# Optimization experiments

Hardware: AMD Instinct MI355X
Metric: run time of the kernel (lower is better)

Reference implementation:

```python
import jax, jax.numpy as jnp
import numpy as np

B, N = 4, 4096
CIN, COUT = 64, 64
K, R, BOX = 3, 32, 4
MLP = COUT * 4
HEADS = 4
EPS = 0.0


def setup_inputs() -> dict:
    key = jax.random.key(0)
    ks = jax.random.split(key, 16)
    s = lambda i, shape: jax.random.normal(ks[i], shape, jnp.float32) * 0.05
    return dict(
        features=jax.random.normal(ks[0], (B, CIN, N), jnp.float32),
        coords=jax.random.normal(ks[1], (B, 3, N), jnp.float32),
        conv_w=s(2, (COUT, CIN, K, K, K)), conv_b=jnp.zeros((COUT,), jnp.float32),
        ln1_g=jnp.ones((COUT,), jnp.float32), ln1_b=jnp.zeros((COUT,), jnp.float32),
        qkv_w=s(3, (3 * COUT, COUT)), qkv_b=jnp.zeros((3 * COUT,), jnp.float32),
        proj_w=s(4, (COUT, COUT)), proj_b=jnp.zeros((COUT,), jnp.float32),
        ln2_g=jnp.ones((COUT,), jnp.float32), ln2_b=jnp.zeros((COUT,), jnp.float32),
        mlp_w1=s(5, (MLP, COUT)), mlp_b1=jnp.zeros((MLP,), jnp.float32),
        mlp_w2=s(6, (COUT, MLP)), mlp_b2=jnp.zeros((COUT,), jnp.float32),
        se_w1=s(7, (COUT // 8, COUT)), se_w2=s(8, (COUT, COUT // 8)),
        pt_in_w=s(9, (COUT, CIN)), pt_in_b=jnp.zeros((COUT,), jnp.float32),
        q_w=s(10, (COUT // 4, COUT)), k_w=s(11, (COUT // 4, COUT)),
        v_w=s(12, (COUT, COUT)),
        trans_w=s(13, (COUT, COUT)), trans_b=jnp.zeros((COUT,), jnp.float32),
    )


def layernorm(x, g, b):
    m = x.mean(-1, keepdims=True)
    v = x.var(-1, keepdims=True)
    return (x - m) * jax.lax.rsqrt(v + 1e-5) * g + b


def voxelize(features, coords):
    # PVCNN-style: center, normalize to [0,1], scale to [0, R-1]; scatter-mean.
    c = coords - coords.mean(axis=2, keepdims=True)  # (B,3,N)
    mx = jnp.sqrt((c ** 2).sum(axis=1, keepdims=True)).max(axis=2, keepdims=True)
    nc = c / (2.0 * mx + EPS) + 0.5
    nc = jnp.clip(nc * R, 0.0, R - 1)  # float coords in [0, R-1]
    vc = jnp.round(nc).astype(jnp.int32)
    idx = (vc[:, 0] * R + vc[:, 1]) * R + vc[:, 2]
    idx = (idx + jnp.arange(B, dtype=jnp.int32)[:, None] * R ** 3).reshape(-1)
    flat = features.transpose(0, 2, 1).reshape(B * N, CIN)
    sums = jax.ops.segment_sum(flat, idx, num_segments=B * R ** 3)
    cnt = jax.ops.segment_sum(jnp.ones((B * N,), jnp.float32), idx, num_segments=B * R ** 3)
    avg = sums / jnp.maximum(cnt, 1.0)[:, None]
    grid = avg.reshape(B, R, R, R, CIN).transpose(0, 4, 1, 2, 3)  # (B,C,R,R,R)
    return grid, nc


def devoxelize(grid, nc):
    # trilinear gather from (B,C,R,R,R) at float coords nc (B,3,N)
    g = grid.reshape(B, COUT, R ** 3)
    x0 = jnp.floor(nc)
    f = nc - x0
    x0 = x0.astype(jnp.int32)
    out = jnp.zeros((B, COUT, N), jnp.float32)
    for dx in (0, 1):
        for dy in (0, 1):
            for dz in (0, 1):
                xi = jnp.clip(x0[:, 0] + dx, 0, R - 1)
                yi = jnp.clip(x0[:, 1] + dy, 0, R - 1)
                zi = jnp.clip(x0[:, 2] + dz, 0, R - 1)
                idx = (xi * R + yi) * R + zi  # (B,N)
                w = ((f[:, 0] if dx else 1 - f[:, 0]) *
                     (f[:, 1] if dy else 1 - f[:, 1]) *
                     (f[:, 2] if dz else 1 - f[:, 2]))
                vals = jnp.take_along_axis(g, jnp.broadcast_to(idx[:, None, :], (B, COUT, N)), axis=2)
                out = out + vals * w[:, None, :]
    return out


def voxel_encoder(grid, conv_w, conv_b, ln1_g, ln1_b, qkv_w, qkv_b, proj_w, proj_b,
                  ln2_g, ln2_b, mlp_w1, mlp_b1, mlp_w2, mlp_b2):
    x = jax.lax.conv_general_dilated(grid, conv_w, (1, 1, 1), 'SAME',
                                     dimension_numbers=('NCDHW', 'OIDHW', 'NCDHW'))
    x = jax.nn.relu(x + conv_b[None, :, None, None, None])
    nb = R // BOX
    # window partition -> (B*nb^3, BOX^3, C)
    t = x.transpose(0, 2, 3, 4, 1).reshape(B, nb, BOX, nb, BOX, nb, BOX, COUT)
    t = t.transpose(0, 1, 3, 5, 2, 4, 6, 7).reshape(B * nb ** 3, BOX ** 3, COUT)
    h = layernorm(t, ln1_g, ln1_b)
    qkv = h @ qkv_w.T + qkv_b
    q, k, v = jnp.split(qkv, 3, axis=-1)
    hd = COUT // HEADS
    sh = lambda z: z.reshape(z.shape[0], z.shape[1], HEADS, hd).transpose(0, 2, 1, 3)
    q, k, v = sh(q), sh(k), sh(v)
    attn = jax.nn.softmax(jnp.einsum('whid,whjd->whij', q, k) / np.float32(np.sqrt(hd)), axis=-1)
    o = jnp.einsum('whij,whjd->whid', attn, v).transpose(0, 2, 1, 3).reshape(t.shape)
    t = t + (o @ proj_w.T + proj_b)
    h = layernorm(t, ln2_g, ln2_b)
    t = t + (jax.nn.gelu(h @ mlp_w1.T + mlp_b1) @ mlp_w2.T + mlp_b2)
    t = t.reshape(B, nb, nb, nb, BOX, BOX, BOX, COUT)
    t = t.transpose(0, 1, 4, 2, 5, 3, 6, 7).reshape(B, R, R, R, COUT)
    return t.transpose(0, 4, 1, 2, 3)


def se3d(x, w1, w2):
    s = x.mean(axis=(2, 3, 4))  # (B,C)
    s = jax.nn.sigmoid(jax.nn.relu(s @ w1.T) @ w2.T)
    return x * s[:, :, None, None, None]


def point_branch(features, pt_in_w, pt_in_b, q_w, k_w, v_w, trans_w, trans_b):
    # PCT-style offset self-attention over points (shared transformer)
    x = jax.nn.relu(jnp.einsum('oc,bcn->bon', pt_in_w, features) + pt_in_b[None, :, None])
    q = jnp.einsum('dc,bcn->bdn', q_w, x)
    k = jnp.einsum('dc,bcn->bdn', k_w, x)
    v = jnp.einsum('oc,bcn->bon', v_w, x)
    attn = jax.nn.softmax(jnp.einsum('bdn,bdm->bnm', q, k) / np.float32(np.sqrt(q.shape[1])), axis=-1)
    o = jnp.einsum('bom,bnm->bon', v, attn)
    off = jax.nn.relu(jnp.einsum('oc,bcn->bon', trans_w, x - o) + trans_b[None, :, None])
    return x + off


def reference(features, coords, conv_w, conv_b, ln1_g, ln1_b, qkv_w, qkv_b, proj_w, proj_b,
              ln2_g, ln2_b, mlp_w1, mlp_b1, mlp_w2, mlp_b2, se_w1, se_w2,
              pt_in_w, pt_in_b, q_w, k_w, v_w, trans_w, trans_b):
    grid, nc = voxelize(features, coords)
    vf = voxel_encoder(grid, conv_w, conv_b, ln1_g, ln1_b, qkv_w, qkv_b, proj_w, proj_b,
                       ln2_g, ln2_b, mlp_w1, mlp_b1, mlp_w2, mlp_b2)
    vf = se3d(vf, se_w1, se_w2)
    vf = devoxelize(vf, nc)
    fused = vf + point_branch(features, pt_in_w, pt_in_b, q_w, k_w, v_w, trans_w, trans_b)
    return fused, coords
```

## Files before the change

kernel.cpp:

```cpp
#include <hip/hip_runtime.h>

#define BN 4
#define NP 4096
#define RV 32
#define VX (RV*RV*RV)

typedef __attribute__((ext_vector_type(8))) short bf16x8;
typedef __attribute__((ext_vector_type(4))) float f32x4;

__device__ __forceinline__ float bf2f(unsigned short u){
  union{unsigned u;float f;}v; v.u=((unsigned)u)<<16; return v.f; }
__device__ __forceinline__ unsigned short f2bf(float f){
  union{float f;unsigned u;}v; v.f=f; unsigned r=v.u + 0x7fffu + ((v.u>>16)&1u);
  return (unsigned short)(r>>16); }
__device__ __forceinline__ unsigned pack2bf(float a, float b){
  return (unsigned)f2bf(a) | ((unsigned)f2bf(b) << 16); }

union ABu { uint4 u; bf16x8 v; };

__global__ void stats_kernel(const float* __restrict__ coords, float* __restrict__ stats)
{
  __shared__ float red[256];
  __shared__ float mean[3];
  const int b = blockIdx.x;
  const int tid = threadIdx.x;
  float s0=0.f,s1=0.f,s2=0.f;
  for (int n = tid; n < NP; n += 256) {
    s0 += coords[((size_t)(b*3)+0)*NP + n];
    s1 += coords[((size_t)(b*3)+1)*NP + n];
    s2 += coords[((size_t)(b*3)+2)*NP + n];
  }
  float sv[3] = {s0,s1,s2};
  for (int ax = 0; ax < 3; ax++) {
    __syncthreads();
    red[tid] = sv[ax];
    __syncthreads();
    for (int st = 128; st > 0; st >>= 1) {
// ... 65 lines not shown
  #pragma unroll
  for (int j = 0; j < 8; j++) {
    int i = c16*8 + j;
    wpre[dst + j] = f2bf(wt[(o*64 + i)*27 + tap]);
  }
}

__global__ void eprep_kernel(const float* __restrict__ qkv_w, const float* __restrict__ proj_w,
                             const float* __restrict__ w1, const float* __restrict__ w2,
                             unsigned short* __restrict__ dst)
{
  int t = blockIdx.x*256 + threadIdx.x;
  float v;
  if (t < 12288)      v = qkv_w[t];
  else if (t < 16384) v = proj_w[t-12288];
  else if (t < 32768) v = w1[t-16384];
  else                v = w2[t-32768];
  dst[t] = f2bf(v);
}

__global__ __launch_bounds__(256) void conv_mfma_kernel(
    const float* __restrict__ sums, const float* __restrict__ cnt,
    const unsigned short* __restrict__ wpre,
    const float* __restrict__ bias, float* __restrict__ gout)
{
  __shared__ uint4 plane[6*34*8];
  __shared__ uint4 wsm[3*64*8];
  const int tid = threadIdx.x;
  const int blk = blockIdx.x;
  const int yq = blk & 7, z = (blk >> 3) & 31, b = blk >> 8;
  const int y0 = yq * 4;
  const int w  = tid >> 6;
  const int lm = tid & 15;
  const int kg = (tid >> 4) & 3;

  f32x4 acc[2][4];
  #pragma unroll
  for (int mt = 0; mt < 2; mt++)
    #pragma unroll
    for (int nt = 0; nt < 4; nt++)
      #pragma unroll
      for (int r = 0; r < 4; r++) acc[mt][nt][r] = 0.f;

  float bv[4];
  #pragma unroll
  for (int nt = 0; nt < 4; nt++) bv[nt] = bias[nt*16 + lm];

// ... 39 lines not shown
          const int wsz = cb ^ (lm & 7);
          w0.u = wsm[(kw*64 +      lm)*8 + wsz];
          w1.u = wsm[(kw*64 + 16 + lm)*8 + wsz];
          w2.u = wsm[(kw*64 + 32 + lm)*8 + wsz];
          w3.u = wsm[(kw*64 + 48 + lm)*8 + wsz];
          acc[0][0] = __builtin_amdgcn_mfma_f32_16x16x32_bf16(a0.v, w0.v, acc[0][0], 0,0,0);
          acc[1][0] = __builtin_amdgcn_mfma_f32_16x16x32_bf16(a1.v, w0.v, acc[1][0], 0,0,0);
          acc[0][1] = __builtin_amdgcn_mfma_f32_16x16x32_bf16(a0.v, w1.v, acc[0][1], 0,0,0);
          acc[1][1] = __builtin_amdgcn_mfma_f32_16x16x32_bf16(a1.v, w1.v, acc[1][1], 0,0,0);
          acc[0][2] = __builtin_amdgcn_mfma_f32_16x16x32_bf16(a0.v, w2.v, acc[0][2], 0,0,0);
          acc[1][2] = __builtin_amdgcn_mfma_f32_16x16x32_bf16(a1.v, w2.v, acc[1][2], 0,0,0);
          acc[0][3] = __builtin_amdgcn_mfma_f32_16x16x32_bf16(a0.v, w3.v, acc[0][3], 0,0,0);
          acc[1][3] = __builtin_amdgcn_mfma_f32_16x16x32_bf16(a1.v, w3.v, acc[1][3], 0,0,0);
        }
      }
    }
  }
  const int y = y0 + w;
  #pragma unroll
  for (int mt = 0; mt < 2; mt++) {
    #pragma unroll
    for (int r = 0; r < 4; r++) {
      const int x = mt*16 + kg*4 + r;
      float* dst = gout + ((size_t)(b*VX) + (z*32 + y)*32 + x)*64 + lm;
      #pragma unroll
      for (int nt = 0; nt < 4; nt++)
        dst[nt*16] = fmaxf(acc[mt][nt][r] + bv[nt], 0.f);
    }
  }
}

__global__ __launch_bounds__(256) void encoder_kernel(
    float* __restrict__ grid,
    const float* __restrict__ ln1_g, const float* __restrict__ ln1_b,
    const float* __restrict__ qkv_b, const float* __restrict__ proj_b,
    const float* __restrict__ ln2_g, const float* __restrict__ ln2_b,
    const float* __restrict__ b1, const float* __restrict__ b2,
    const unsigned short* __restrict__ encw,
    float* __restrict__ se_sum)
{
  __shared__ float t_s[64*65];
  __shared__ unsigned short aT[64*72];
  __shared__ unsigned short qk[4*64*72];
  __shared__ float mean_s[64], rstd_s[64];
  __shared__ float sered[256];
  unsigned short* q_s = qk;
  unsigned short* k_s = qk + 4608;
  unsigned short* v_s = qk + 9216;
  unsigned short* o_s = qk + 13824;
  unsigned short* hid = qk;
  unsigned short* p_s = aT;

  const unsigned short* wqb = encw;
  const unsigned short* wpb = encw + 12288;
  const unsigned short* w1b = encw + 16384;
  const unsigned short* w2b = encw + 32768;

  const int tid = threadIdx.x;
  const int w = tid >> 6;
  const int lane = tid & 63;
  const int cl = lane & 15;
  const int quad = lane >> 4;
  const int win = blockIdx.x;
  const int b = win >> 9, wn = win & 511;
  const int zb = wn >> 6, yb = (wn >> 3) & 7, xb = wn & 7;
  const size_t gb = (size_t)b * VX * 64;

  for (int e = tid; e < 4096; e += 256) {
    int tok = e >> 6, c = e & 63;
    int zl = tok >> 4, yl = (tok >> 2) & 3, xl = tok & 3;
    int vox = ((zb*4+zl)*32 + (yb*4+yl))*32 + (xb*4+xl);
    t_s[tok*65 + c] = grid[gb + (size_t)vox*64 + c];
  }
  __syncthreads();
  {
    int i = tid >> 2, part = tid & 3;
    float sum = 0.f, sq = 0.f;
    for (int c = part; c < 64; c += 4) { float x = t_s[i*65+c]; sum += x; sq += x*x; }
    sum += __shfl_xor(sum, 1); sq += __shfl_xor(sq, 1);
    sum += __shfl_xor(sum, 2); sq += __shfl_xor(sq, 2);
    if (part == 0) {
      float m = sum * (1.f/64.f);
      float var = sq * (1.f/64.f) - m*m;
      mean_s[i] = m; rstd_s[i] = rsqrtf(var + 1e-5f);
    }
  }
  __syncthreads();
  for (int e = tid; e < 4096; e += 256) {
    int tok = e >> 6, c = e & 63;
    float h = (t_s[tok*65+c] - mean_s[tok]) * rstd_s[tok] * ln1_g[c] + ln1_b[c];
    aT[tok*72 + c] = f2bf(h);
  }
  __syncthreads();
  {
    #pragma unroll
    for (int ci = 0; ci < 3; ci++) {
      const int d0 = 48*w + ci*16;
      ABu a0, a1;
      a0.u = *(const uint4*)(wqb + (d0 + cl)*64 + quad*8);
      a1.u = *(const uint4*)(wqb + (d0 + cl)*64 + 32 + quad*8);
      float4 bias4 = *(const float4*)(qkv_b + d0 + quad*4);
      #pragma unroll
      for (int tt = 0; tt < 4; tt++) {
        ABu h0, h1;
        h0.u = *(const uint4*)(aT + (tt*16 + cl)*72 + quad*8);
        h1.u = *(const uint4*)(aT + (tt*16 + cl)*72 + 32 + quad*8);
        f32x4 d = {0.f,0.f,0.f,0.f};
        d = __builtin_amdgcn_mfma_f32_16x16x32_bf16(a0.v, h0.v, d, 0,0,0);
        d = __builtin_amdgcn_mfma_f32_16x16x32_bf16(a1.v, h1.v, d, 0,0,0);
        if (d0 < 64) {
          unsigned lo = pack2bf((d[0]+bias4.x)*0.25f, (d[1]+bias4.y)*0.25f);
          unsigned hi = pack2bf((d[2]+bias4.z)*0.25f, (d[3]+bias4.w)*0.25f);
          *(uint2*)(q_s + (tt*16+cl)*72 + d0 + quad*4) = make_uint2(lo, hi);
        } else if (d0 < 128) {
          unsigned lo = pack2bf(d[0]+bias4.x, d[1]+bias4.y);
          unsigned hi = pack2bf(d[2]+bias4.z, d[3]+bias4.w);
          *(uint2*)(k_s + (tt*16+cl)*72 + (d0-64) + quad*4) = make_uint2(lo, hi);
        } else {
          const float* bp = (const float*)&bias4;
          #pragma unroll
          for (int r = 0; r < 4; r++)
            v_s[((d0-128) + quad*4 + r)*72 + tt*16 + cl] = f2bf(d[r] + bp[r]);
        }
      }
    }
  }
  __syncthreads();
  {
    const uint4 z4 = make_uint4(0u,0u,0u,0u);
    #pragma unroll
    for (int h = 0; h < 4; h++) {
      const int hb = h*16;
      ABu bq;
      if (quad < 2) bq.u = *(const uint4*)(q_s + (w*16 + cl)*72 + hb + quad*8);
      else bq.u = z4;
      float sc[4][4];
      #pragma unroll
      for (int tj = 0; tj < 4; tj++) {
        ABu ak;
        if (quad < 2) ak.u = *(const uint4*)(k_s + (tj*16 + cl)*72 + hb + quad*8);
        else ak.u = z4;
        f32x4 d = {0.f,0.f,0.f,0.f};
        d = __builtin_amdgcn_mfma_f32_16x16x32_bf16(ak.v, bq.v, d, 0,0,0);
        #pragma unroll
        for (int r = 0; r < 4; r++) sc[tj][r] = d[r];
      }
      float mx = -1e30f;
      #pragma unroll
      for (int tj = 0; tj < 4; tj++)
        #pragma unroll
        for (int r = 0; r < 4; r++) mx = fmaxf(mx, sc[tj][r]);
      mx = fmaxf(mx, __shfl_xor(mx, 16));
      mx = fmaxf(mx, __shfl_xor(mx, 32));
      float psum = 0.f;
      #pragma unroll
      for (int tj = 0; tj < 4; tj++) {
        float p0 = __expf(sc[tj][0]-mx), p1 = __expf(sc[tj][1]-mx);
        float p2 = __expf(sc[tj][2]-mx), p3 = __expf(sc[tj][3]-mx);
        psum += p0+p1+p2+p3;
        *(uint2*)(p_s + (w*16+cl)*72 + tj*16 + quad*4) =
            make_uint2(pack2bf(p0,p1), pack2bf(p2,p3));
      }
      psum += __shfl_xor(psum, 16);
      psum += __shfl_xor(psum, 32);
      float inv = 1.f / psum;
      f32x4 oacc = {0.f,0.f,0.f,0.f};
      #pragma unroll
      for (int kk = 0; kk < 2; kk++) {
        ABu av, bp;
        av.u = *(const uint4*)(v_s + (hb + cl)*72 + kk*32 + quad*8);
        bp.u = *(const uint4*)(p_s + (w*16 + cl)*72 + kk*32 + quad*8);
        oacc = __builtin_amdgcn_mfma_f32_16x16x32_bf16(av.v, bp.v, oacc, 0,0,0);
      }
      *(uint2*)(o_s + (w*16+cl)*72 + hb + quad*4) =
          make_uint2(pack2bf(oacc[0]*inv, oacc[1]*inv), pack2bf(oacc[2]*inv, oacc[3]*inv));
    }
  }
  __syncthreads();
  {
    const int c0 = w*16;
    ABu a0, a1;
    a0.u = *(const uint4*)(wpb + (c0 + cl)*64 + quad*8);
    a1.u = *(const uint4*)(wpb + (c0 + cl)*64 + 32 + quad*8);
    float4 pb4 = *(const float4*)(proj_b + c0 + quad*4);
    const float* pbp = (const float*)&pb4;
    #pragma unroll
    for (int tt = 0; tt < 4; tt++) {
      ABu o0, o1;
      o0.u = *(const uint4*)(o_s + (tt*16 + cl)*72 + quad*8);
      o1.u = *(const uint4*)(o_s + (tt*16 + cl)*72 + 32 + quad*8);
      f32x4 d = {0.f,0.f,0.f,0.f};
      d = __builtin_amdgcn_mfma_f32_16x16x32_bf16(a0.v, o0.v, d, 0,0,0);
      d = __builtin_amdgcn_mfma_f32_16x16x32_bf16(a1.v, o1.v, d, 0,0,0);
      #pragma unroll
      for (int r = 0; r < 4; r++)
        t_s[(tt*16+cl)*65 + c0 + quad*4 + r] += d[r] + pbp[r];
    }
  }
  __syncthreads();
  {
    int i = tid >> 2, part = tid & 3;
    float sum = 0.f, sq = 0.f;
    for (int c = part; c < 64; c += 4) { float x = t_s[i*65+c]; sum += x; sq += x*x; }
    sum += __shfl_xor(sum, 1); sq += __shfl_xor(sq, 1);
    sum += __shfl_xor(sum, 2); sq += __shfl_xor(sq, 2);
    if (part == 0) {
      float m = sum * (1.f/64.f);
      float var = sq * (1.f/64.f) - m*m;
      mean_s[i] = m; rstd_s[i] = rsqrtf(var + 1e-5f);
    }
  }
  __syncthreads();
  for (int e = tid; e < 4096; e += 256) {
    int tok = e >> 6, c = e & 63;
    float h = (t_s[tok*65+c] - mean_s[tok]) * rstd_s[tok] * ln2_g[c] + ln2_b[c];
    aT[tok*72 + c] = f2bf(h);
  }
  __syncthreads();
  {
    const int m0w = w*64;
    ABu hb0[4], hb1[4];
    #pragma unroll
    for (int tt = 0; tt < 4; tt++) {
      hb0[tt].u = *(const uint4*)(aT + (tt*16 + cl)*72 + quad*8);
      hb1[tt].u = *(const uint4*)(aT + (tt*16 + cl)*72 + 32 + quad*8);
    }
    f32x4 acc1[4][4];
    #pragma unroll
    for (int mt = 0; mt < 4; mt++) {
      ABu a0, a1;
      a0.u = *(const uint4*)(w1b + (m0w + mt*16 + cl)*64 + quad*8);
      a1.u = *(const uint4*)(w1b + (m0w + mt*16 + cl)*64 + 32 + quad*8);
      #pragma unroll
      for (int tt = 0; tt < 4; tt++) {
        f32x4 d = {0.f,0.f,0.f,0.f};
        d = __builtin_amdgcn_mfma_f32_16x16x32_bf16(a0.v, hb0[tt].v, d, 0,0,0);
        d = __builtin_amdgcn_mfma_f32_16x16x32_bf16(a1.v, hb1[tt].v, d, 0,0,0);
        acc1[mt][tt] = d;
      }
    }
    __syncthreads();
    #pragma unroll
    for (int mt = 0; mt < 4; mt++) {
      float4 b14 = *(const float4*)(b1 + m0w + mt*16 + quad*4);
      const float* bp = (const float*)&b14;
      #pragma unroll
      for (int tt = 0; tt < 4; tt++) {
        float g[4];
        #pragma unroll
        for (int r = 0; r < 4; r++) {
          float x = acc1[mt][tt][r] + bp[r];
          float u = 1.5957691f * (x + 0.044715f*x*x*x);
          g[r] = x / (1.f + __expf(-u));
        }
        *(uint2*)(hid + (tt*16+cl)*264 + m0w + mt*16 + quad*4) =
            make_uint2(pack2bf(g[0],g[1]), pack2bf(g[2],g[3]));
      }
    }
  }
  __syncthreads();
  {
    const int c0 = w*16;
    f32x4 acc2[4];
    #pragma unroll
    for (int tt = 0; tt < 4; tt++)
      #pragma unroll
      for (int r = 0; r < 4; r++) acc2[tt][r] = 0.f;
    #pragma unroll
    for (int kk = 0; kk < 8; kk++) {
      ABu a;
      a.u = *(const uint4*)(w2b + (c0 + cl)*256 + kk*32 + quad*8);
      #pragma unroll
      for (int tt = 0; tt < 4; tt++) {
        ABu bh;
        bh.u = *(const uint4*)(hid + (tt*16 + cl)*264 + kk*32 + quad*8);
        acc2[tt] = __builtin_amdgcn_mfma_f32_16x16x32_bf16(a.v, bh.v, acc2[tt], 0,0,0);
      }
    }
    float4 b24 = *(const float4*)(b2 + c0 + quad*4);
    const float* bp = (const float*)&b24;
    #pragma unroll
    for (int tt = 0; tt < 4; tt++)
      #pragma unroll
      for (int r = 0; r < 4; r++)
        t_s[(tt*16+cl)*65 + c0 + quad*4 + r] += acc2[tt][r] + bp[r];
  }
  __syncthreads();
  for (int e = tid; e < 4096; e += 256) {
    int tok = e >> 6, c = e & 63;
    int zl = tok >> 4, yl = (tok >> 2) & 3, xl = tok & 3;
    int vox = ((zb*4+zl)*32 + (yb*4+yl))*32 + (xb*4+xl);
    grid[gb + (size_t)vox*64 + c] = t_s[tok*65 + c];
  }
  {
    int c = tid & 63, quarter = tid >> 6;
    float ps = 0.f;
    #pragma unroll
    for (int t = 0; t < 16; t++) ps += t_s[(quarter*16+t)*65 + c];
    sered[quarter*64 + c] = ps;
  }
  __syncthreads();
  if (tid < 64)
    atomicAdd(&se_sum[b*64 + tid],
              sered[tid] + sered[64+tid] + sered[128+tid] + sered[192+tid]);
}

__global__ void se_kernel(const float* __restrict__ se_sum, const float* __restrict__ w1,
                          const float* __restrict__ w2, float* __restrict__ scale)
{
  __shared__ float mean_s[256];
  __shared__ float z1[32];
  int tid = threadIdx.x;
  mean_s[tid] = se_sum[tid] * (1.f / VX);
  __syncthreads();
  if (tid < 32) {
    int bb = tid >> 3, j = tid & 7;
    float a = 0.f;
    for (int c = 0; c < 64; c++) a += mean_s[bb*64 + c] * w1[j*64 + c];
    z1[tid] = fmaxf(a, 0.f);
  }
  __syncthreads();
// ... 57 lines not shown
  }
  if (tid < 128) {
    int d = tid & 15, which = (tid >> 4) & 1, g2 = tid >> 5;
    int t0b = g2 * 16;
    const float* wp = which ? k_w : q_w;
    float scl = which ? 1.f : 0.25f;
    float acc[16];
    #pragma unroll
    for (int t = 0; t < 16; t++) acc[t] = 0.f;
    for (int cc = 0; cc < 64; cc++) {
      float wv = wp[d*64 + cc];
      #pragma unroll
      for (int t = 0; t < 16; t++) acc[t] += x_s[(t0b+t)*65 + cc] * wv;
    }
    unsigned short* dst = which ? k_bf : q_bf;
    #pragma unroll
    for (int t = 0; t < 16; t++)
      dst[((size_t)(b*NP) + n0 + t0b + t)*16 + d] = f2bf(acc[t] * scl);
  }
}

__global__ __launch_bounds__(256) void point_attn_kernel(
    const unsigned short* __restrict__ q_bf, const unsigned short* __restrict__ k_bf,
    const unsigned short* __restrict__ v_tt, float* __restrict__ o_t)
{
  __shared__ unsigned short q_s[64*24];
  __shared__ unsigned short k_sh[2][64*24];
  __shared__ unsigned short v_sh[2][64*72];
  __shared__ unsigned short p_s[64*72];
  const int tid = threadIdx.x;
  const int b = blockIdx.x >> 6;
  const int n0 = (blockIdx.x & 63) * 64;
  const int w = tid >> 6;
  const int lane = tid & 63;
  const int cl = lane & 15;
  const int quad = lane >> 4;
  const uint4 z4 = make_uint4(0u,0u,0u,0u);

  const unsigned* qbu = (const unsigned*)q_bf;
  const unsigned* kbu = (const unsigned*)k_bf;
  const unsigned* vtu = (const unsigned*)v_tt;
  unsigned* q_su = (unsigned*)q_s;

  {
    unsigned* kd = (unsigned*)k_sh[0];
    unsigned* vd = (unsigned*)v_sh[0];
    for (int e = tid; e < 512; e += 256) {
      int tok = e >> 3, du = e & 7;
      q_su[tok*12 + du] = qbu[((size_t)(b*NP) + n0 + tok)*8 + du];
      kd[tok*12 + du]   = kbu[((size_t)(b*NP) + tok)*8 + du];
    }
    for (int e = tid; e < 2048; e += 256) {
      int cc = e >> 5, tu = e & 31;
      vd[cc*36 + tu] = vtu[((size_t)(b*64) + cc)*2048 + tu];
    }
  }
  float m_run = -1e30f, l_run = 0.f;
  f32x4 acc[4];
  #pragma unroll
  for (int ct = 0; ct < 4; ct++)
    #pragma unroll
    for (int r = 0; r < 4; r++) acc[ct][r] = 0.f;
  __syncthreads();

  ABu bq;
  if (quad < 2) bq.u = *(const uint4*)(q_s + (w*16 + cl)*24 + quad*8);
  else bq.u = z4;

  for (int t = 0; t < 64; t++) {
    const int cur = t & 1;
    unsigned pk[2], pv[8];
    if (t+1 < 64) {
      const int m1 = (t+1)*64;
      #pragma unroll
      for (int i = 0; i < 2; i++) {
        int e = tid + i*256;
        pk[i] = kbu[((size_t)(b*NP) + m1 + (e>>3))*8 + (e&7)];
      }
      #pragma unroll
      for (int i = 0; i < 8; i++) {
        int e = tid + i*256;
        pv[i] = vtu[((size_t)(b*64) + (e>>5))*2048 + (m1>>1) + (e&31)];
      }
    }
    const unsigned short* ks = k_sh[cur];
    const unsigned short* vs = v_sh[cur];
    float sc[4][4];
    #pragma unroll
    for (int tj = 0; tj < 4; tj++) {
      ABu ak;
      if (quad < 2) ak.u = *(const uint4*)(ks + (tj*16 + cl)*24 + quad*8);
      else ak.u = z4;
      f32x4 d = {0.f,0.f,0.f,0.f};
      d = __builtin_amdgcn_mfma_f32_16x16x32_bf16(ak.v, bq.v, d, 0,0,0);
      #pragma unroll
// ... 17 lines not shown
      *(uint2*)(p_s + (w*16+cl)*72 + tj*16 + quad*4) =
          make_uint2(pack2bf(p0,p1), pack2bf(p2,p3));
    }
    psum += __shfl_xor(psum, 16);
    psum += __shfl_xor(psum, 32);
    l_run = l_run*alpha + psum;
    m_run = mnew;
    #pragma unroll
    for (int ct = 0; ct < 4; ct++)
      #pragma unroll
      for (int r = 0; r < 4; r++) acc[ct][r] *= alpha;
    #pragma unroll
    for (int kk = 0; kk < 2; kk++) {
      ABu bp;
      bp.u = *(const uint4*)(p_s + (w*16 + cl)*72 + kk*32 + quad*8);
      #pragma unroll
      for (int ct = 0; ct < 4; ct++) {
        ABu av;
        av.u = *(const uint4*)(vs + (ct*16 + cl)*72 + kk*32 + quad*8);
        acc[ct] = __builtin_amdgcn_mfma_f32_16x16x32_bf16(av.v, bp.v, acc[ct], 0,0,0);
      }
    }
    __syncthreads();
    if (t+1 < 64) {
      unsigned* kd = (unsigned*)k_sh[1-cur];
      unsigned* vd = (unsigned*)v_sh[1-cur];
      #pragma unroll
      for (int i = 0; i < 2; i++) {
        int e = tid + i*256;
        kd[(e>>3)*12 + (e&7)] = pk[i];
      }
      #pragma unroll
      for (int i = 0; i < 8; i++) {
        int e = tid + i*256;
        vd[(e>>5)*36 + (e&31)] = pv[i];
      }
    }
    __syncthreads();
  }
  const float inv = 1.f / l_run;
  const int tok = n0 + w*16 + cl;
  #pragma unroll
  for (int ct = 0; ct < 4; ct++) {
    float4 o4;
    o4.x = acc[ct][0]*inv; o4.y = acc[ct][1]*inv;
    o4.z = acc[ct][2]*inv; o4.w = acc[ct][3]*inv;
    *(float4*)&o_t[((size_t)(b*NP) + tok)*64 + ct*16 + quad*4] = o4;
  }
}

__global__ __launch_bounds__(256) void fuse_kernel(
    const float* __restrict__ x_t, const float* __restrict__ o_t,
    const float* __restrict__ trans_w, const float* __restrict__ trans_b,
    const float* __restrict__ grid, const float* __restrict__ se_scale,
    const float* __restrict__ nc, float* __restrict__ out)
{
  __shared__ float tw_s[64*65];
  __shared__ float d_s[64*65];
  __shared__ float r_s[64*65];
  const int tid = threadIdx.x;
  const int blk = blockIdx.x;
  const int b = blk >> 6;
  const int n0 = (blk & 63) * 64;
  for (int e = tid; e < 4096; e += 256) {
    int c = e >> 6, k = e & 63;
    tw_s[c*65 + k] = trans_w[e];
  }
  for (int e = tid; e < 4096; e += 256) {
    int nl = e >> 6, c = e & 63;
    size_t idx = ((size_t)(b*NP) + n0 + nl)*64 + c;
    d_s[nl*65 + c] = x_t[idx] - o_t[idx];
  }
  __syncthreads();
  const int cl = tid & 63, g = tid >> 6;
  const float ses = se_scale[b*64 + cl];
  const float tb = trans_b[cl];
  for (int t = 0; t < 16; t++) {
    int nl = g*16 + t;
    int n = n0 + nl;
    float off = 0.f;
    for (int k = 0; k < 64; k++) off += tw_s[cl*65 + k] * d_s[nl*65 + k];
    off = fmaxf(off + tb, 0.f);
    float ncx = nc[((size_t)(b*3)+0)*NP + n];
    float ncy = nc[((size_t)(b*3)+1)*NP + n];
    float ncz = nc[((size_t)(b*3)+2)*NP + n];
    float fx0 = floorf(ncx), fy0 = floorf(ncy), fz0 = floorf(ncz);
    int x0 = (int)fx0, y0 = (int)fy0, z0 = (int)fz0;
    float fx = ncx - fx0, fy = ncy - fy0, fz = ncz - fz0;
    float wx[2] = {1.f-fx, fx}, wy[2] = {1.f-fy, fy}, wz[2] = {1.f-fz, fz};
    float vf = 0.f;
    #pragma unroll
    for (int cor = 0; cor < 8; cor++) {
      int dx = cor >> 2, dy = (cor >> 1) & 1, dz = cor & 1;
      int xi = min(x0+dx, 31), yi = min(y0+dy, 31), zi = min(z0+dz, 31);
      float wgt = wx[dx]*wy[dy]*wz[dz];
      vf += wgt * grid[((size_t)(b*VX) + (xi*32+yi)*32 + zi)*64 + cl];
    }
    vf *= ses;
    float xval = x_t[((size_t)(b*NP) + n)*64 + cl];
    r_s[cl*65 + nl] = xval + off + vf;
  }
  __syncthreads();
  for (int e = tid; e < 4096; e += 256) {
    int c = e >> 6, nl = e & 63;
    out[((size_t)(b*64) + c)*NP + n0 + nl] = r_s[c*65 + nl];
  }
}

extern "C" void kernel_launch(void* const* d_in, const int* in_sizes, int n_in,
                              void* d_out, int out_size, void* d_ws, size_t ws_size,
                              hipStream_t stream)
{
  const float* features = (const float*)d_in[0];
  const float* coords   = (const float*)d_in[1];
  const float* conv_w   = (const float*)d_in[2];
  const float* conv_b   = (const float*)d_in[3];
  const float* ln1_g    = (const float*)d_in[4];
  const float* ln1_b    = (const float*)d_in[5];
  const float* qkv_w    = (const float*)d_in[6];
  const float* qkv_b    = (const float*)d_in[7];
  const float* proj_w   = (const float*)d_in[8];
  const float* proj_b   = (const float*)d_in[9];
  const float* ln2_g    = (const float*)d_in[10];
  const float* ln2_b    = (const float*)d_in[11];
  const float* mlp_w1   = (const float*)d_in[12];
  const float* mlp_b1   = (const float*)d_in[13];
  const float* mlp_w2   = (const float*)d_in[14];
  const float* mlp_b2   = (const float*)d_in[15];
  const float* se_w1    = (const float*)d_in[16];
  const float* se_w2    = (const float*)d_in[17];
  const float* pt_in_w  = (const float*)d_in[18];
  const float* pt_in_b  = (const float*)d_in[19];
  const float* q_w      = (const float*)d_in[20];
  const float* k_w      = (const float*)d_in[21];
  const float* v_w      = (const float*)d_in[22];
  const float* v_trans_w= (const float*)d_in[23];
  const float* v_trans_b= (const float*)d_in[24];

  char* ws = (char*)d_ws;
  float* stats    = (float*)(ws + 0);
  float* se_sum   = (float*)(ws + 256);
  float* se_scale = (float*)(ws + 1280);
  float* nc       = (float*)(ws + 4096);
  float* cnt      = (float*)(ws + 200704);
  float* grid0    = (float*)(ws + 724992);
  float* grid1    = (float*)(ws + 34279424);
  float* x_t = (float*)(ws + 724992);
  unsigned short* q_bf = (unsigned short*)(ws + 724992 + 4194304);
  unsigned short* k_bf = (unsigned short*)(ws + 724992 + 5242880);
  unsigned short* v_tt = (unsigned short*)(ws + 724992 + 6291456);
  float* o_t = (float*)(ws + 724992 + 10485760);
  unsigned short* wpre = (unsigned short*)d_out;
  unsigned short* encw = (unsigned short*)((char*)d_out + 221184);

  hipMemsetAsync(se_sum, 0, 1024, stream);
  hipMemsetAsync(cnt, 0, 524288 + 33554432, stream);

  wprep_kernel<<<54, 256, 0, stream>>>(conv_w, wpre);
  eprep_kernel<<<192, 256, 0, stream>>>(qkv_w, proj_w, mlp_w1, mlp_w2, encw);
  stats_kernel<<<BN, 256, 0, stream>>>(coords, stats);
  scatter_kernel<<<256, 256, 0, stream>>>(features, coords, stats, nc, grid0, cnt);
  conv_mfma_kernel<<<1024, 256, 0, stream>>>(grid0, cnt, wpre, conv_b, grid1);
  encoder_kernel<<<2048, 256, 0, stream>>>(grid1, ln1_g, ln1_b, qkv_b, proj_b,
      ln2_g, ln2_b, mlp_b1, mlp_b2, encw, se_sum);
  se_kernel<<<1, 256, 0, stream>>>(se_sum, se_w1, se_w2, se_scale);
  point_in_kernel<<<256, 256, 0, stream>>>(features, pt_in_w, pt_in_b, q_w, k_w, v_w,
      x_t, q_bf, k_bf, v_tt);
  point_attn_kernel<<<256, 256, 0, stream>>>(q_bf, k_bf, v_tt, o_t);
  fuse_kernel<<<256, 256, 0, stream>>>(x_t, o_t, v_trans_w, v_trans_b, grid1,
      se_scale, nc, (float*)d_out);
  hipMemcpyAsync((char*)d_out + (size_t)BN*64*NP*4, coords, (size_t)BN*3*NP*4,
                 hipMemcpyDeviceToDevice, stream);
}
```

Before: 475.8 us.

## Split point attention over keys, store voxel grid in bf16, shrink encoder LDS

Point attention now runs split-K: each of 4 blocks per query tile handles a quarter of the keys and writes unnormalized partials plus max/sum, which the fuse kernel merges. This raises the block count from 256 to 1024 to fill the CUs. The conv output grid and the encoder's residual stream are stored in bf16 to halve global and LDS traffic. The encoder's MLP hidden layer is processed in 64-wide chunks to cut LDS usage, likely raising occupancy. The fuse kernel uses 32-point tiles with twice as many blocks. The bf16 residual storage adds rounding error, and the split-K partials add extra global traffic.

```diff
diff --git a/kernel.cpp b/kernel.cpp
--- a/kernel.cpp
+++ b/kernel.cpp
@@ -13,6 +13,9 @@
 __device__ __forceinline__ unsigned short f2bf(float f){
   union{float f;unsigned u;}v; v.f=f; unsigned r=v.u + 0x7fffu + ((v.u>>16)&1u);
   return (unsigned short)(r>>16); }
+__device__ __forceinline__ float2 bfp2f2(unsigned p){
+  union{unsigned u;float f;}a,b; a.u=p<<16; b.u=p&0xffff0000u;
+  float2 r; r.x=a.f; r.y=b.f; return r; }
 __device__ __forceinline__ unsigned pack2bf(float a, float b){
   return (unsigned)f2bf(a) | ((unsigned)f2bf(b) << 16); }
 
@@ -124,7 +127,7 @@
 __global__ __launch_bounds__(256) void conv_mfma_kernel(
     const float* __restrict__ sums, const float* __restrict__ cnt,
     const unsigned short* __restrict__ wpre,
-    const float* __restrict__ bias, float* __restrict__ gout)
+    const float* __restrict__ bias, unsigned short* __restrict__ gout)
 {
   __shared__ uint4 plane[6*34*8];
   __shared__ uint4 wsm[3*64*8];
@@ -210,16 +213,16 @@
     #pragma unroll
     for (int r = 0; r < 4; r++) {
       const int x = mt*16 + kg*4 + r;
-      float* dst = gout + ((size_t)(b*VX) + (z*32 + y)*32 + x)*64 + lm;
+      unsigned short* dst = gout + ((size_t)(b*VX) + (z*32 + y)*32 + x)*64 + lm;
       #pragma unroll
       for (int nt = 0; nt < 4; nt++)
-        dst[nt*16] = fmaxf(acc[mt][nt][r] + bv[nt], 0.f);
+        dst[nt*16] = f2bf(fmaxf(acc[mt][nt][r] + bv[nt], 0.f));
     }
   }
 }
 
 __global__ __launch_bounds__(256) void encoder_kernel(
-    float* __restrict__ grid,
+    unsigned short* __restrict__ grid,
     const float* __restrict__ ln1_g, const float* __restrict__ ln1_b,
     const float* __restrict__ qkv_b, const float* __restrict__ proj_b,
     const float* __restrict__ ln2_g, const float* __restrict__ ln2_b,
@@ -227,17 +230,13 @@
     const unsigned short* __restrict__ encw,
     float* __restrict__ se_sum)
 {
-  __shared__ float t_s[64*65];
-  __shared__ unsigned short aT[64*72];
-  __shared__ unsigned short qk[4*64*72];
+  __shared__ unsigned short t_b[64*72];
+  __shared__ unsigned short h_b[64*72];
+  __shared__ unsigned short q_b[64*72];
+  __shared__ unsigned short k_b[64*72];
+  __shared__ unsigned short v_b[64*72];
   __shared__ float mean_s[64], rstd_s[64];
   __shared__ float sered[256];
-  unsigned short* q_s = qk;
-  unsigned short* k_s = qk + 4608;
-  unsigned short* v_s = qk + 9216;
-  unsigned short* o_s = qk + 13824;
-  unsigned short* hid = qk;
-  unsigned short* p_s = aT;
 
   const unsigned short* wqb = encw;
   const unsigned short* wpb = encw + 12288;
@@ -254,17 +253,17 @@
   const int zb = wn >> 6, yb = (wn >> 3) & 7, xb = wn & 7;
   const size_t gb = (size_t)b * VX * 64;
 
-  for (int e = tid; e < 4096; e += 256) {
-    int tok = e >> 6, c = e & 63;
+  for (int e = tid; e < 1024; e += 256) {
+    int tok = e >> 4, cg = e & 15;
     int zl = tok >> 4, yl = (tok >> 2) & 3, xl = tok & 3;
     int vox = ((zb*4+zl)*32 + (yb*4+yl))*32 + (xb*4+xl);
-    t_s[tok*65 + c] = grid[gb + (size_t)vox*64 + c];
+    *(uint2*)(t_b + tok*72 + cg*4) = *(const uint2*)(grid + gb + (size_t)vox*64 + cg*4);
   }
   __syncthreads();
   {
     int i = tid >> 2, part = tid & 3;
     float sum = 0.f, sq = 0.f;
-    for (int c = part; c < 64; c += 4) { float x = t_s[i*65+c]; sum += x; sq += x*x; }
+    for (int c = part; c < 64; c += 4) { float x = bf2f(t_b[i*72+c]); sum += x; sq += x*x; }
     sum += __shfl_xor(sum, 1); sq += __shfl_xor(sq, 1);
     sum += __shfl_xor(sum, 2); sq += __shfl_xor(sq, 2);
     if (part == 0) {
@@ -276,8 +275,8 @@
   __syncthreads();
   for (int e = tid; e < 4096; e += 256) {
     int tok = e >> 6, c = e & 63;
-    float h = (t_s[tok*65+c] - mean_s[tok]) * rstd_s[tok] * ln1_g[c] + ln1_b[c];
-    aT[tok*72 + c] = f2bf(h);
+    float h = (bf2f(t_b[tok*72+c]) - mean_s[tok]) * rstd_s[tok] * ln1_g[c] + ln1_b[c];
+    h_b[tok*72 + c] = f2bf(h);
   }
   __syncthreads();
   {
@@ -291,42 +290,43 @@
       #pragma unroll
       for (int tt = 0; tt < 4; tt++) {
         ABu h0, h1;
-        h0.u = *(const uint4*)(aT + (tt*16 + cl)*72 + quad*8);
-        h1.u = *(const uint4*)(aT + (tt*16 + cl)*72 + 32 + quad*8);
+        h0.u = *(const uint4*)(h_b + (tt*16 + cl)*72 + quad*8);
+        h1.u = *(const uint4*)(h_b + (tt*16 + cl)*72 + 32 + quad*8);
         f32x4 d = {0.f,0.f,0.f,0.f};
         d = __builtin_amdgcn_mfma_f32_16x16x32_bf16(a0.v, h0.v, d, 0,0,0);
         d = __builtin_amdgcn_mfma_f32_16x16x32_bf16(a1.v, h1.v, d, 0,0,0);
         if (d0 < 64) {
-          unsigned lo = pack2bf((d[0]+bias4.x)*0.25f, (d[1]+bias4.y)*0.25f);
-          unsigned hi = pack2bf((d[2]+bias4.z)*0.25f, (d[3]+bias4.w)*0.25f);
-          *(uint2*)(q_s + (tt*16+cl)*72 + d0 + quad*4) = make_uint2(lo, hi);
+          *(uint2*)(q_b + (tt*16+cl)*72 + d0 + quad*4) =
+            make_uint2(pack2bf((d[0]+bias4.x)*0.25f, (d[1]+bias4.y)*0.25f),
+                       pack2bf((d[2]+bias4.z)*0.25f, (d[3]+bias4.w)*0.25f));
         } else if (d0 < 128) {
-          unsigned lo = pack2bf(d[0]+bias4.x, d[1]+bias4.y);
-          unsigned hi = pack2bf(d[2]+bias4.z, d[3]+bias4.w);
-          *(uint2*)(k_s + (tt*16+cl)*72 + (d0-64) + quad*4) = make_uint2(lo, hi);
+          *(uint2*)(k_b + (tt*16+cl)*72 + (d0-64) + quad*4) =
+            make_uint2(pack2bf(d[0]+bias4.x, d[1]+bias4.y),
+                       pack2bf(d[2]+bias4.z, d[3]+bias4.w));
         } else {
           const float* bp = (const float*)&bias4;
           #pragma unroll
           for (int r = 0; r < 4; r++)
-            v_s[((d0-128) + quad*4 + r)*72 + tt*16 + cl] = f2bf(d[r] + bp[r]);
+            v_b[((d0-128) + quad*4 + r)*72 + tt*16 + cl] = f2bf(d[r] + bp[r]);
         }
       }
     }
   }
   __syncthreads();
+  uint2 pk[4];
   {
     const uint4 z4 = make_uint4(0u,0u,0u,0u);
     #pragma unroll
     for (int h = 0; h < 4; h++) {
       const int hb = h*16;
       ABu bq;
-      if (quad < 2) bq.u = *(const uint4*)(q_s + (w*16 + cl)*72 + hb + quad*8);
+      if (quad < 2) bq.u = *(const uint4*)(q_b + (w*16 + cl)*72 + hb + quad*8);
       else bq.u = z4;
       float sc[4][4];
       #pragma unroll
       for (int tj = 0; tj < 4; tj++) {
         ABu ak;
-        if (quad < 2) ak.u = *(const uint4*)(k_s + (tj*16 + cl)*72 + hb + quad*8);
+        if (quad < 2) ak.u = *(const uint4*)(k_b + (tj*16 + cl)*72 + hb + quad*8);
         else ak.u = z4;
         f32x4 d = {0.f,0.f,0.f,0.f};
         d = __builtin_amdgcn_mfma_f32_16x16x32_bf16(ak.v, bq.v, d, 0,0,0);
@@ -346,7 +346,7 @@
         float p0 = __expf(sc[tj][0]-mx), p1 = __expf(sc[tj][1]-mx);
         float p2 = __expf(sc[tj][2]-mx), p3 = __expf(sc[tj][3]-mx);
         psum += p0+p1+p2+p3;
-        *(uint2*)(p_s + (w*16+cl)*72 + tj*16 + quad*4) =
+        *(uint2*)(h_b + (w*16+cl)*72 + tj*16 + quad*4) =
             make_uint2(pack2bf(p0,p1), pack2bf(p2,p3));
       }
       psum += __shfl_xor(psum, 16);
@@ -356,14 +356,18 @@
       #pragma unroll
       for (int kk = 0; kk < 2; kk++) {
         ABu av, bp;
-        av.u = *(const uint4*)(v_s + (hb + cl)*72 + kk*32 + quad*8);
-        bp.u = *(const uint4*)(p_s + (w*16 + cl)*72 + kk*32 + quad*8);
+        av.u = *(const uint4*)(v_b + (hb + cl)*72 + kk*32 + quad*8);
+        bp.u = *(const uint4*)(h_b + (w*16 + cl)*72 + kk*32 + quad*8);
         oacc = __builtin_amdgcn_mfma_f32_16x16x32_bf16(av.v, bp.v, oacc, 0,0,0);
       }
-      *(uint2*)(o_s + (w*16+cl)*72 + hb + quad*4) =
-          make_uint2(pack2bf(oacc[0]*inv, oacc[1]*inv), pack2bf(oacc[2]*inv, oacc[3]*inv));
-    }
-  }
+      pk[h] = make_uint2(pack2bf(oacc[0]*inv, oacc[1]*inv),
+                         pack2bf(oacc[2]*inv, oacc[3]*inv));
+    }
+  }
+  __syncthreads();
+  #pragma unroll
+  for (int h = 0; h < 4; h++)
+    *(uint2*)(k_b + (w*16+cl)*72 + h*16 + quad*4) = pk[h];
   __syncthreads();
   {
     const int c0 = w*16;
@@ -371,25 +375,26 @@
     a0.u = *(const uint4*)(wpb + (c0 + cl)*64 + quad*8);
     a1.u = *(const uint4*)(wpb + (c0 + cl)*64 + 32 + quad*8);
     float4 pb4 = *(const float4*)(proj_b + c0 + quad*4);
-    const float* pbp = (const float*)&pb4;
     #pragma unroll
     for (int tt = 0; tt < 4; tt++) {
       ABu o0, o1;
-      o0.u = *(const uint4*)(o_s + (tt*16 + cl)*72 + quad*8);
-      o1.u = *(const uint4*)(o_s + (tt*16 + cl)*72 + 32 + quad*8);
+      o0.u = *(const uint4*)(k_b + (tt*16 + cl)*72 + quad*8);
+      o1.u = *(const uint4*)(k_b + (tt*16 + cl)*72 + 32 + quad*8);
       f32x4 d = {0.f,0.f,0.f,0.f};
       d = __builtin_amdgcn_mfma_f32_16x16x32_bf16(a0.v, o0.v, d, 0,0,0);
       d = __builtin_amdgcn_mfma_f32_16x16x32_bf16(a1.v, o1.v, d, 0,0,0);
-      #pragma unroll
-      for (int r = 0; r < 4; r++)
-        t_s[(tt*16+cl)*65 + c0 + quad*4 + r] += d[r] + pbp[r];
+      uint2* tp = (uint2*)(t_b + (tt*16+cl)*72 + c0 + quad*4);
+      uint2 told = *tp;
+      float2 t01 = bfp2f2(told.x), t23 = bfp2f2(told.y);
+      *tp = make_uint2(pack2bf(t01.x + d[0] + pb4.x, t01.y + d[1] + pb4.y),
+                       pack2bf(t23.x + d[2] + pb4.z, t23.y + d[3] + pb4.w));
     }
   }
   __syncthreads();
   {
     int i = tid >> 2, part = tid & 3;
     float sum = 0.f, sq = 0.f;
-    for (int c = part; c < 64; c += 4) { float x = t_s[i*65+c]; sum += x; sq += x*x; }
+    for (int c = part; c < 64; c += 4) { float x = bf2f(t_b[i*72+c]); sum += x; sq += x*x; }
     sum += __shfl_xor(sum, 1); sq += __shfl_xor(sq, 1);
     sum += __shfl_xor(sum, 2); sq += __shfl_xor(sq, 2);
     if (part == 0) {
@@ -401,90 +406,81 @@
   __syncthreads();
   for (int e = tid; e < 4096; e += 256) {
     int tok = e >> 6, c = e & 63;
-    float h = (t_s[tok*65+c] - mean_s[tok]) * rstd_s[tok] * ln2_g[c] + ln2_b[c];
-    aT[tok*72 + c] = f2bf(h);
-  }
-  __syncthreads();
-  {
-    const int m0w = w*64;
+    float h = (bf2f(t_b[tok*72+c]) - mean_s[tok]) * rstd_s[tok] * ln2_g[c] + ln2_b[c];
+    h_b[tok*72 + c] = f2bf(h);
+  }
+  __syncthreads();
+  {
+    const int c0 = w*16;
     ABu hb0[4], hb1[4];
     #pragma unroll
     for (int tt = 0; tt < 4; tt++) {
-      hb0[tt].u = *(const uint4*)(aT + (tt*16 + cl)*72 + quad*8);
-      hb1[tt].u = *(const uint4*)(aT + (tt*16 + cl)*72 + 32 + quad*8);
-    }
-    f32x4 acc1[4][4];
-    #pragma unroll
-    for (int mt = 0; mt < 4; mt++) {
+      hb0[tt].u = *(const uint4*)(h_b + (tt*16 + cl)*72 + quad*8);
+      hb1[tt].u = *(const uint4*)(h_b + (tt*16 + cl)*72 + 32 + quad*8);
+    }
+    f32x4 acc2[4];
+    #pragma unroll
+    for (int tt = 0; tt < 4; tt++)
+      #pragma unroll
+      for (int r = 0; r < 4; r++) acc2[tt][r] = 0.f;
+    for (int ch = 0; ch < 4; ch++) {
+      const int m0 = ch*64 + w*16;
       ABu a0, a1;
-      a0.u = *(const uint4*)(w1b + (m0w + mt*16 + cl)*64 + quad*8);
-      a1.u = *(const uint4*)(w1b + (m0w + mt*16 + cl)*64 + 32 + quad*8);
+      a0.u = *(const uint4*)(w1b + (m0 + cl)*64 + quad*8);
+      a1.u = *(const uint4*)(w1b + (m0 + cl)*64 + 32 + quad*8);
+      float4 b14 = *(const float4*)(b1 + m0 + quad*4);
+      const float* bp = (const float*)&b14;
       #pragma unroll
       for (int tt = 0; tt < 4; tt++) {
         f32x4 d = {0.f,0.f,0.f,0.f};
         d = __builtin_amdgcn_mfma_f32_16x16x32_bf16(a0.v, hb0[tt].v, d, 0,0,0);
         d = __builtin_amdgcn_mfma_f32_16x16x32_bf16(a1.v, hb1[tt].v, d, 0,0,0);
-        acc1[mt][tt] = d;
-      }
-    }
-    __syncthreads();
-    #pragma unroll
-    for (int mt = 0; mt < 4; mt++) {
-      float4 b14 = *(const float4*)(b1 + m0w + mt*16 + quad*4);
-      const float* bp = (const float*)&b14;
-      #pragma unroll
-      for (int tt = 0; tt < 4; tt++) {
         float g[4];
         #pragma unroll
         for (int r = 0; r < 4; r++) {
-          float x = acc1[mt][tt][r] + bp[r];
+          float x = d[r] + bp[r];
           float u = 1.5957691f * (x + 0.044715f*x*x*x);
           g[r] = x / (1.f + __expf(-u));
         }
-        *(uint2*)(hid + (tt*16+cl)*264 + m0w + mt*16 + quad*4) =
+        *(uint2*)(q_b + (tt*16+cl)*72 + w*16 + quad*4) =
             make_uint2(pack2bf(g[0],g[1]), pack2bf(g[2],g[3]));
       }
-    }
-  }
-  __syncthreads();
-  {
-    const int c0 = w*16;
-    f32x4 acc2[4];
-    #pragma unroll
-    for (int tt = 0; tt < 4; tt++)
-      #pragma unroll
-      for (int r = 0; r < 4; r++) acc2[tt][r] = 0.f;
-    #pragma unroll
-    for (int kk = 0; kk < 8; kk++) {
-      ABu a;
-      a.u = *(const uint4*)(w2b + (c0 + cl)*256 + kk*32 + quad*8);
+      __syncthreads();
+      ABu a20, a21;
+      a20.u = *(const uint4*)(w2b + (c0 + cl)*256 + ch*64 + quad*8);
+      a21.u = *(const uint4*)(w2b + (c0 + cl)*256 + ch*64 + 32 + quad*8);
       #pragma unroll
       for (int tt = 0; tt < 4; tt++) {
-        ABu bh;
-        bh.u = *(const uint4*)(hid + (tt*16 + cl)*264 + kk*32 + quad*8);
-        acc2[tt] = __builtin_amdgcn_mfma_f32_16x16x32_bf16(a.v, bh.v, acc2[tt], 0,0,0);
-      }
+        ABu bh0, bh1;
+        bh0.u = *(const uint4*)(q_b + (tt*16 + cl)*72 + quad*8);
+        bh1.u = *(const uint4*)(q_b + (tt*16 + cl)*72 + 32 + quad*8);
+        acc2[tt] = __builtin_amdgcn_mfma_f32_16x16x32_bf16(a20.v, bh0.v, acc2[tt], 0,0,0);
+        acc2[tt] = __builtin_amdgcn_mfma_f32_16x16x32_bf16(a21.v, bh1.v, acc2[tt], 0,0,0);
+      }
+      __syncthreads();
     }
     float4 b24 = *(const float4*)(b2 + c0 + quad*4);
-    const float* bp = (const float*)&b24;
-    #pragma unroll
-    for (int tt = 0; tt < 4; tt++)
-      #pragma unroll
-      for (int r = 0; r < 4; r++)
-        t_s[(tt*16+cl)*65 + c0 + quad*4 + r] += acc2[tt][r] + bp[r];
-  }
-  __syncthreads();
-  for (int e = tid; e < 4096; e += 256) {
-    int tok = e >> 6, c = e & 63;
+    #pragma unroll
+    for (int tt = 0; tt < 4; tt++) {
+      uint2* tp = (uint2*)(t_b + (tt*16+cl)*72 + c0 + quad*4);
+      uint2 told = *tp;
+      float2 t01 = bfp2f2(told.x), t23 = bfp2f2(told.y);
+      *tp = make_uint2(pack2bf(t01.x + acc2[tt][0] + b24.x, t01.y + acc2[tt][1] + b24.y),
+                       pack2bf(t23.x + acc2[tt][2] + b24.z, t23.y + acc2[tt][3] + b24.w));
+    }
+  }
+  __syncthreads();
+  for (int e = tid; e < 1024; e += 256) {
+    int tok = e >> 4, cg = e & 15;
     int zl = tok >> 4, yl = (tok >> 2) & 3, xl = tok & 3;
     int vox = ((zb*4+zl)*32 + (yb*4+yl))*32 + (xb*4+xl);
-    grid[gb + (size_t)vox*64 + c] = t_s[tok*65 + c];
+    *(uint2*)(grid + gb + (size_t)vox*64 + cg*4) = *(const uint2*)(t_b + tok*72 + cg*4);
   }
   {
     int c = tid & 63, quarter = tid >> 6;
     float ps = 0.f;
     #pragma unroll
-    for (int t = 0; t < 16; t++) ps += t_s[(quarter*16+t)*65 + c];
+    for (int t = 0; t < 16; t++) ps += bf2f(t_b[(quarter*16+t)*72 + c]);
     sered[quarter*64 + c] = ps;
   }
   __syncthreads();
@@ -588,15 +584,20 @@
 
 __global__ __launch_bounds__(256) void point_attn_kernel(
     const unsigned short* __restrict__ q_bf, const unsigned short* __restrict__ k_bf,
-    const unsigned short* __restrict__ v_tt, float* __restrict__ o_t)
+    const unsigned short* __restrict__ v_tt,
+    float* __restrict__ opart, float2* __restrict__ mlbuf)
 {
   __shared__ unsigned short q_s[64*24];
   __shared__ unsigned short k_sh[2][64*24];
   __shared__ unsigned short v_sh[2][64*72];
   __shared__ unsigned short p_s[64*72];
   const int tid = threadIdx.x;
-  const int b = blockIdx.x >> 6;
-  const int n0 = (blockIdx.x & 63) * 64;
+  const int blk = blockIdx.x;
+  const int b = blk >> 8;
+  const int nb = (blk >> 2) & 63;
+  const int s = blk & 3;
+  const int n0 = nb * 64;
+  const int t_beg = s*16, t_end = s*16 + 16;
   const int w = tid >> 6;
   const int lane = tid & 63;
   const int cl = lane & 15;
@@ -614,11 +615,11 @@
     for (int e = tid; e < 512; e += 256) {
       int tok = e >> 3, du = e & 7;
       q_su[tok*12 + du] = qbu[((size_t)(b*NP) + n0 + tok)*8 + du];
-      kd[tok*12 + du]   = kbu[((size_t)(b*NP) + tok)*8 + du];
+      kd[tok*12 + du]   = kbu[((size_t)(b*NP) + t_beg*64 + tok)*8 + du];
     }
     for (int e = tid; e < 2048; e += 256) {
       int cc = e >> 5, tu = e & 31;
-      vd[cc*36 + tu] = vtu[((size_t)(b*64) + cc)*2048 + tu];
+      vd[cc*36 + tu] = vtu[((size_t)(b*64) + cc)*2048 + t_beg*32 + tu];
     }
   }
   float m_run = -1e30f, l_run = 0.f;
@@ -633,10 +634,10 @@
   if (quad < 2) bq.u = *(const uint4*)(q_s + (w*16 + cl)*24 + quad*8);
   else bq.u = z4;
 
-  for (int t = 0; t < 64; t++) {
+  for (int t = t_beg; t < t_end; t++) {
     const int cur = t & 1;
     unsigned pk[2], pv[8];
-    if (t+1 < 64) {
+    if (t+1 < t_end) {
       const int m1 = (t+1)*64;
       #pragma unroll
       for (int i = 0; i < 2; i++) {
@@ -700,7 +701,7 @@
       }
     }
     __syncthreads();
-    if (t+1 < 64) {
+    if (t+1 < t_end) {
       unsigned* kd = (unsigned*)k_sh[1-cur];
       unsigned* vd = (unsigned*)v_sh[1-cur];
       #pragma unroll
@@ -716,45 +717,70 @@
     }
     __syncthreads();
   }
-  const float inv = 1.f / l_run;
   const int tok = n0 + w*16 + cl;
   #pragma unroll
   for (int ct = 0; ct < 4; ct++) {
     float4 o4;
-    o4.x = acc[ct][0]*inv; o4.y = acc[ct][1]*inv;
-    o4.z = acc[ct][2]*inv; o4.w = acc[ct][3]*inv;
-    *(float4*)&o_t[((size_t)(b*NP) + tok)*64 + ct*16 + quad*4] = o4;
-  }
+    o4.x = acc[ct][0]; o4.y = acc[ct][1]; o4.z = acc[ct][2]; o4.w = acc[ct][3];
+    *(float4*)&opart[(((size_t)(s*BN + b))*NP + tok)*64 + ct*16 + quad*4] = o4;
+  }
+  if (quad == 0)
+    mlbuf[(size_t)(s*BN + b)*NP + tok] = make_float2(m_run, l_run);
 }
 
 __global__ __launch_bounds__(256) void fuse_kernel(
-    const float* __restrict__ x_t, const float* __restrict__ o_t,
+    const float* __restrict__ x_t, const float* __restrict__ opart,
+    const float2* __restrict__ mlbuf,
     const float* __restrict__ trans_w, const float* __restrict__ trans_b,
-    const float* __restrict__ grid, const float* __restrict__ se_scale,
+    const unsigned short* __restrict__ grid, const float* __restrict__ se_scale,
     const float* __restrict__ nc, float* __restrict__ out)
 {
   __shared__ float tw_s[64*65];
-  __shared__ float d_s[64*65];
-  __shared__ float r_s[64*65];
+  __shared__ float d_s[32*65];
+  __shared__ float r_s[64*33];
+  __shared__ float mw[32][6];
   const int tid = threadIdx.x;
   const int blk = blockIdx.x;
-  const int b = blk >> 6;
-  const int n0 = (blk & 63) * 64;
+  const int b = blk >> 7;
+  const int n0 = (blk & 127) * 32;
   for (int e = tid; e < 4096; e += 256) {
     int c = e >> 6, k = e & 63;
     tw_s[c*65 + k] = trans_w[e];
   }
-  for (int e = tid; e < 4096; e += 256) {
+  if (tid < 32) {
+    int nl = tid;
+    float m[4], l[4];
+    #pragma unroll
+    for (int s = 0; s < 4; s++) {
+      float2 v = mlbuf[(size_t)(s*BN + b)*NP + n0 + nl];
+      m[s] = v.x; l[s] = v.y;
+    }
+    float M = fmaxf(fmaxf(m[0], m[1]), fmaxf(m[2], m[3]));
+    float L = 0.f;
+    #pragma unroll
+    for (int s = 0; s < 4; s++) {
+      float ws = __expf(m[s] - M);
+      mw[nl][s] = ws;
+      L += l[s] * ws;
+    }
+    mw[nl][4] = 1.f / L;
+  }
+  __syncthreads();
+  for (int e = tid; e < 2048; e += 256) {
     int nl = e >> 6, c = e & 63;
-    size_t idx = ((size_t)(b*NP) + n0 + nl)*64 + c;
-    d_s[nl*65 + c] = x_t[idx] - o_t[idx];
+    size_t pbase = ((size_t)(b*NP) + n0 + nl)*64 + c;
+    const size_t sstr = (size_t)BN*NP*64;
+    float o = opart[pbase]        * mw[nl][0] + opart[pbase +   sstr] * mw[nl][1]
+            + opart[pbase+2*sstr] * mw[nl][2] + opart[pbase + 3*sstr] * mw[nl][3];
+    o *= mw[nl][4];
+    d_s[nl*65 + c] = x_t[pbase] - o;
   }
   __syncthreads();
   const int cl = tid & 63, g = tid >> 6;
   const float ses = se_scale[b*64 + cl];
   const float tb = trans_b[cl];
-  for (int t = 0; t < 16; t++) {
-    int nl = g*16 + t;
+  for (int t = 0; t < 8; t++) {
+    int nl = g*8 + t;
     int n = n0 + nl;
     float off = 0.f;
     for (int k = 0; k < 64; k++) off += tw_s[cl*65 + k] * d_s[nl*65 + k];
@@ -772,16 +798,16 @@
       int dx = cor >> 2, dy = (cor >> 1) & 1, dz = cor & 1;
       int xi = min(x0+dx, 31), yi = min(y0+dy, 31), zi = min(z0+dz, 31);
       float wgt = wx[dx]*wy[dy]*wz[dz];
-      vf += wgt * grid[((size_t)(b*VX) + (xi*32+yi)*32 + zi)*64 + cl];
+      vf += wgt * bf2f(grid[((size_t)(b*VX) + (xi*32+yi)*32 + zi)*64 + cl]);
     }
     vf *= ses;
     float xval = x_t[((size_t)(b*NP) + n)*64 + cl];
-    r_s[cl*65 + nl] = xval + off + vf;
-  }
-  __syncthreads();
-  for (int e = tid; e < 4096; e += 256) {
-    int c = e >> 6, nl = e & 63;
-    out[((size_t)(b*64) + c)*NP + n0 + nl] = r_s[c*65 + nl];
+    r_s[cl*33 + nl] = xval + off + vf;
+  }
+  __syncthreads();
+  for (int e = tid; e < 2048; e += 256) {
+    int c = e >> 5, nl = e & 31;
+    out[((size_t)(b*64) + c)*NP + n0 + nl] = r_s[c*33 + nl];
   }
 }
 
@@ -822,12 +848,13 @@
   float* nc       = (float*)(ws + 4096);
   float* cnt      = (float*)(ws + 200704);
   float* grid0    = (float*)(ws + 724992);
-  float* grid1    = (float*)(ws + 34279424);
+  unsigned short* grid1b = (unsigned short*)(ws + 34279424);
   float* x_t = (float*)(ws + 724992);
   unsigned short* q_bf = (unsigned short*)(ws + 724992 + 4194304);
   unsigned short* k_bf = (unsigned short*)(ws + 724992 + 5242880);
   unsigned short* v_tt = (unsigned short*)(ws + 724992 + 6291456);
-  float* o_t = (float*)(ws + 724992 + 10485760);
+  float*  opart = (float*)(ws + 724992 + 10485760);
+  float2* mlbuf = (float2*)(ws + 724992 + 27787264);
   unsigned short* wpre = (unsigned short*)d_out;
   unsigned short* encw = (unsigned short*)((char*)d_out + 221184);
 
@@ -838,15 +865,15 @@
   eprep_kernel<<<192, 256, 0, stream>>>(qkv_w, proj_w, mlp_w1, mlp_w2, encw);
   stats_kernel<<<BN, 256, 0, stream>>>(coords, stats);
   scatter_kernel<<<256, 256, 0, stream>>>(features, coords, stats, nc, grid0, cnt);
-  conv_mfma_kernel<<<1024, 256, 0, stream>>>(grid0, cnt, wpre, conv_b, grid1);
-  encoder_kernel<<<2048, 256, 0, stream>>>(grid1, ln1_g, ln1_b, qkv_b, proj_b,
+  conv_mfma_kernel<<<1024, 256, 0, stream>>>(grid0, cnt, wpre, conv_b, grid1b);
+  encoder_kernel<<<2048, 256, 0, stream>>>(grid1b, ln1_g, ln1_b, qkv_b, proj_b,
       ln2_g, ln2_b, mlp_b1, mlp_b2, encw, se_sum);
   se_kernel<<<1, 256, 0, stream>>>(se_sum, se_w1, se_w2, se_scale);
   point_in_kernel<<<256, 256, 0, stream>>>(features, pt_in_w, pt_in_b, q_w, k_w, v_w,
       x_t, q_bf, k_bf, v_tt);
-  point_attn_kernel<<<256, 256, 0, stream>>>(q_bf, k_bf, v_tt, o_t);
-  fuse_kernel<<<256, 256, 0, stream>>>(x_t, o_t, v_trans_w, v_trans_b, grid1,
-      se_scale, nc, (float*)d_out);
+  point_attn_kernel<<<1024, 256, 0, stream>>>(q_bf, k_bf, v_tt, opart, mlbuf);
+  fuse_kernel<<<512, 256, 0, stream>>>(x_t, opart, mlbuf, v_trans_w, v_trans_b,
+      grid1b, se_scale, nc, (float*)d_out);
   hipMemcpyAsync((char*)d_out + (size_t)BN*64*NP*4, coords, (size_t)BN*3*NP*4,
                  hipMemcpyDeviceToDevice, stream);
 }
```

Result: faster. 428.7 us (-9.9%).
